# Optimization experiments

Hardware: AMD Instinct MI355X
Metric: run time of the kernel (lower is better)

The kernel has to match this reference:

```python
import jax, jax.numpy as jnp
import numpy as np

LN_EPS = 1e-5  # torch LayerNorm default
MODES = 4


def setup_inputs() -> dict:
    key = jax.random.key(0)
    ks = jax.random.split(key, 5)
    B, S, H = 4, 4096, 1024
    nh, dk = 16, H // 16
    scale = 1.0 / (H * H)
    # frequency mode selection: random shuffle of range(S//2), take 4, sorted (seeded for determinism)
    rng = np.random.default_rng(0)
    index = jnp.asarray(np.sort(rng.permutation(S // 2)[:MODES]).astype(np.int32))
    return {
        "x": jax.random.normal(ks[0], (B, S, H), dtype=jnp.float32),
        "Wq": jax.random.normal(ks[1], (H, H), dtype=jnp.float32) * np.sqrt(2.0 / (H + dk)),
        "bq": jnp.zeros((H,), dtype=jnp.float32),
        "wr": scale * jax.random.uniform(ks[2], (nh, dk, dk, MODES), dtype=jnp.float32),
        "wi": scale * jax.random.uniform(ks[3], (nh, dk, dk, MODES), dtype=jnp.float32),
        "gamma": jnp.ones((H,), dtype=jnp.float32),
        "beta": jnp.zeros((H,), dtype=jnp.float32),
        "index": index,
    }


def reference(x, Wq, bq, wr, wi, gamma, beta, index):
    B, S, H = x.shape
    nh, dk = wr.shape[0], wr.shape[1]
    # q projection and head split: (B,S,H) -> (B,S,nh,dk) -> (B,nh,dk,S)
    q = (x @ Wq.T + bq).reshape(B, S, nh, dk).transpose(0, 2, 3, 1)
    x_ft = jnp.fft.rfft(q, axis=-1)                 # (B,nh,dk,S//2+1) complex
    xm = x_ft[..., index]                           # gather selected modes: (B,nh,dk,M)
    w = wr + 1j * wi                                # (nh,dk,dk,M) complex
    ym = jnp.einsum('bhim,hiom->bhom', xm, w)       # per-mode complex matmul
    # faithful: results written at slots 0..M-1 of out_ft (loop writes out_ft[...,wi])
    out_ft = jnp.zeros((B, nh, dk, S // 2 + 1), dtype=ym.dtype).at[..., :ym.shape[-1]].set(ym)
    x_if = jnp.fft.irfft(out_ft, n=S, axis=-1)      # (B,nh,dk,S) real
    # faithful permute(0,3,2,1).view: flattens as dk-major over heads
    out = x_if.transpose(0, 3, 2, 1).reshape(B, S, H)
    # dropout is identity in eval mode
    y = out + x
    mu = jnp.mean(y, axis=-1, keepdims=True)
    var = jnp.var(y, axis=-1, keepdims=True)
    return (y - mu) * jax.lax.rsqrt(var + LN_EPS) * gamma + beta
```

## Files before the change

### kernel.cpp

```cpp
#include <hip/hip_runtime.h>
#include <math.h>

#define BB 4
#define SS 4096
#define HH 1024
#define NH 16
#define DK 64
#define NMODES 4
#define NSB 64
#define SCHUNK (SS/NSB)
#define PPLANE ((size_t)BB * NSB * HH)
#define TWO_PI 6.28318530717958647692f

__global__ __launch_bounds__(256) void kA_dft(const float* __restrict__ x,
                                              const int* __restrict__ index,
                                              float* __restrict__ P) {
    __shared__ float tab[SCHUNK * 8];
    int t  = threadIdx.x;
    int sb = blockIdx.x & (NSB - 1);
    int b  = blockIdx.x >> 6;

    {
        int sl = t >> 2, m = t & 3;
        int k  = index[m];
        int sv = sb * SCHUNK + sl;
        int r  = (k * sv) & (SS - 1);
        float ang = (float)r * (TWO_PI / (float)SS);
        float sn, cs;
        sincosf(ang, &sn, &cs);
        tab[sl * 8 + m * 2]     = cs;
        tab[sl * 8 + m * 2 + 1] = sn;
    }
    __syncthreads();

    int c0 = t * 4;
    float acc[4][8];
    #pragma unroll
    for (int e = 0; e < 4; ++e)
        #pragma unroll
        for (int q = 0; q < 8; ++q) acc[e][q] = 0.f;

    const float* xp = x + ((size_t)(b * SS + sb * SCHUNK)) * HH + c0;
    #pragma unroll 4
    for (int r = 0; r < SCHUNK; ++r) {
        float4 xv = *(const float4*)(xp + (size_t)r * HH);
        float4 t0 = *(const float4*)&tab[r * 8];
        float4 t1 = *(const float4*)&tab[r * 8 + 4];
        float xe;
        #pragma unroll
        for (int e = 0; e < 4; ++e) {
            xe = (e == 0) ? xv.x : (e == 1) ? xv.y : (e == 2) ? xv.z : xv.w;
            acc[e][0] += xe * t0.x;  acc[e][1] -= xe * t0.y;
            acc[e][2] += xe * t0.z;  acc[e][3] -= xe * t0.w;
            acc[e][4] += xe * t1.x;  acc[e][5] -= xe * t1.y;
            acc[e][6] += xe * t1.z;  acc[e][7] -= xe * t1.w;
        }
    }
    size_t base = (size_t)(b * NSB + sb) * HH + c0;
    #pragma unroll
    for (int q = 0; q < 8; ++q) {
        *(float4*)&P[q * PPLANE + base] =
            make_float4(acc[0][q], acc[1][q], acc[2][q], acc[3][q]);
    }
}

__global__ __launch_bounds__(256) void kA2_reduce(const float* __restrict__ P,
                                                  float* __restrict__ G) {
    int g = blockIdx.x * 256 + threadIdx.x;
    int j = g & (HH - 1);
    int q = (g >> 10) & 7;
    int b = g >> 13;
    float s = 0.f;
    for (int sb = 0; sb < NSB; ++sb)
        s += P[q * PPLANE + (size_t)(b * NSB + sb) * HH + j];
    G[((size_t)(b * HH + j)) * 8 + q] = s;
}

__global__ __launch_bounds__(256) void kB_proj(const float* __restrict__ Wq,
                                               const float* __restrict__ bq,
                                               const int* __restrict__ index,
                                               const float* __restrict__ G,
                                               float* __restrict__ XM) {
    __shared__ float Gs[HH * 8];
    int t = threadIdx.x;
    int cb = blockIdx.x & 15;
    int b  = blockIdx.x >> 4;
    for (int u = t; u < HH * 8; u += 256) Gs[u] = G[(size_t)b * HH * 8 + u];
    __syncthreads();

    int cl = t >> 2, jq = t & 3;
    int c = cb * 64 + cl;
    float acc[8] = {0.f,0.f,0.f,0.f,0.f,0.f,0.f,0.f};
    for (int j0 = jq * 4; j0 < HH; j0 += 16) {
        float4 wv = *(const float4*)&Wq[(size_t)c * HH + j0];
        const float* gp = &Gs[j0 * 8];
        #pragma unroll
        for (int q = 0; q < 8; ++q) acc[q] += wv.x * gp[q];
        #pragma unroll
        for (int q = 0; q < 8; ++q) acc[q] += wv.y * gp[8 + q];
        #pragma unroll
        for (int q = 0; q < 8; ++q) acc[q] += wv.z * gp[16 + q];
        #pragma unroll
        for (int q = 0; q < 8; ++q) acc[q] += wv.w * gp[24 + q];
    }
    #pragma unroll
    for (int q = 0; q < 8; ++q) {
        acc[q] += __shfl_xor(acc[q], 1);
        acc[q] += __shfl_xor(acc[q], 2);
    }
    if (jq == 0) {
        float bias = bq[c];
        #pragma unroll
        for (int m = 0; m < NMODES; ++m)
            if (index[m] == 0) acc[2 * m] += bias * (float)SS;
        float* o = XM + ((size_t)(b * HH + c)) * 8;
        *(float4*)o       = make_float4(acc[0], acc[1], acc[2], acc[3]);
        *(float4*)(o + 4) = make_float4(acc[4], acc[5], acc[6], acc[7]);
    }
}

#define KC_IQ 8
#define KC_II (DK / KC_IQ)
__global__ __launch_bounds__(512) void kC_modes(const float* __restrict__ wr,
                                                const float* __restrict__ wi,
                                                const float* __restrict__ XM,
                                                float* __restrict__ CF) {
    __shared__ float xs[DK * 8];
    __shared__ float red[KC_IQ][DK][9];
    int t = threadIdx.x;
    int o = t & 63, iq = t >> 6;
    int h = blockIdx.x & 15;
    int b = blockIdx.x >> 4;
    for (int u = t; u < DK * 8; u += 512)
        xs[u] = XM[((size_t)(b * HH + h * DK)) * 8 + u];
    __syncthreads();

    float re[4] = {0.f,0.f,0.f,0.f}, im[4] = {0.f,0.f,0.f,0.f};
    #pragma unroll
    for (int ii = 0; ii < KC_II; ++ii) {
        int i = iq * KC_II + ii;
        float4 wrv = *(const float4*)&wr[(((size_t)(h * DK + i)) * DK + o) * 4];
        float4 wiv = *(const float4*)&wi[(((size_t)(h * DK + i)) * DK + o) * 4];
        float xr, xi;
        xr = xs[i * 8 + 0]; xi = xs[i * 8 + 1];
        re[0] += xr * wrv.x - xi * wiv.x;  im[0] += xr * wiv.x + xi * wrv.x;
        xr = xs[i * 8 + 2]; xi = xs[i * 8 + 3];
        re[1] += xr * wrv.y - xi * wiv.y;  im[1] += xr * wiv.y + xi * wrv.y;
        xr = xs[i * 8 + 4]; xi = xs[i * 8 + 5];
        re[2] += xr * wrv.z - xi * wiv.z;  im[2] += xr * wiv.z + xi * wrv.z;
        xr = xs[i * 8 + 6]; xi = xs[i * 8 + 7];
        re[3] += xr * wrv.w - xi * wiv.w;  im[3] += xr * wiv.w + xi * wrv.w;
    }
    #pragma unroll
    for (int m = 0; m < 4; ++m) {
        red[iq][o][2 * m]     = re[m];
        red[iq][o][2 * m + 1] = im[m];
    }
    __syncthreads();
    if (iq == 0) {
        float rr[8];
        #pragma unroll
        for (int q = 0; q < 8; ++q) {
            float s = 0.f;
            #pragma unroll
            for (int g = 0; g < KC_IQ; ++g) s += red[g][o][q];
            rr[q] = s;
        }
        int co = o * NH + h;
        const float inv = 1.0f / (float)SS;
        float* cp = CF + ((size_t)(b * HH + co)) * 8;
        cp[0] =  rr[0] * inv;
        cp[1] =  2.0f * rr[2] * inv;
        cp[2] = -2.0f * rr[3] * inv;
        cp[3] =  2.0f * rr[4] * inv;
        cp[4] = -2.0f * rr[5] * inv;
        cp[5] =  2.0f * rr[6] * inv;
        cp[6] = -2.0f * rr[7] * inv;
        cp[7] =  0.0f;
    }
}

#define KD_ROWS 16
#define KD_RB 8
__global__ __launch_bounds__(256) void kD_out(const float* __restrict__ x,
                                              const float* __restrict__ CF,
                                              const float* __restrict__ gamma,
                                              const float* __restrict__ beta,
                                              float* __restrict__ out) {
    __shared__ float red[4][KD_RB][2];
    int t  = threadIdx.x;
    int b  = blockIdx.x >> 8;
    int s0 = (blockIdx.x & 255) * KD_ROWS;
    int c0 = t * 4;

    const float* cp = CF + (size_t)b * HH * 8 + (size_t)c0 * 8;
    float4 cfa[8];
    #pragma unroll
    for (int e = 0; e < 4; ++e) {
        cfa[2 * e]     = *(const float4*)(cp + e * 8);
        cfa[2 * e + 1] = *(const float4*)(cp + e * 8 + 4);
    }
    float4 g4 = *(const float4*)&gamma[c0];
    float4 b4 = *(const float4*)&beta[c0];
    int w = t >> 6, lane = t & 63;

    for (int batch = 0; batch < KD_ROWS / KD_RB; ++batch) {
        float y[KD_RB][4], sm[KD_RB], sq[KD_RB];
        #pragma unroll
        for (int r = 0; r < KD_RB; ++r) {
            int s = s0 + batch * KD_RB + r;
            float ang = (float)s * (TWO_PI / (float)SS);
            float s1, c1;
            sincosf(ang, &s1, &c1);
            float c2 = c1 * c1 - s1 * s1, s2 = 2.f * s1 * c1;
            float c3 = c2 * c1 - s2 * s1, s3 = s2 * c1 + c2 * s1;

            float4 xv = *(const float4*)&x[((size_t)(b * SS + s)) * HH + c0];
            #pragma unroll
            for (int e = 0; e < 4; ++e) {
                float xe = (e == 0) ? xv.x : (e == 1) ? xv.y : (e == 2) ? xv.z : xv.w;
                float4 A = cfa[2 * e], Bv = cfa[2 * e + 1];
                y[r][e] = xe + A.x + A.y * c1 + A.z * s1 + A.w * c2
                             + Bv.x * s2 + Bv.y * c3 + Bv.z * s3;
            }
            sm[r] = y[r][0] + y[r][1] + y[r][2] + y[r][3];
            sq[r] = y[r][0]*y[r][0] + y[r][1]*y[r][1]
                  + y[r][2]*y[r][2] + y[r][3]*y[r][3];
        }
        #pragma unroll
        for (int off = 1; off < 64; off <<= 1) {
            #pragma unroll
            for (int r = 0; r < KD_RB; ++r) {
                sm[r] += __shfl_xor(sm[r], off);
                sq[r] += __shfl_xor(sq[r], off);
            }
        }
        if (lane == 0) {
            #pragma unroll
            for (int r = 0; r < KD_RB; ++r) {
                red[w][r][0] = sm[r];
                red[w][r][1] = sq[r];
            }
        }
        __syncthreads();
        #pragma unroll
        for (int r = 0; r < KD_RB; ++r) {
            int s = s0 + batch * KD_RB + r;
            float tot  = red[0][r][0] + red[1][r][0] + red[2][r][0] + red[3][r][0];
            float totq = red[0][r][1] + red[1][r][1] + red[2][r][1] + red[3][r][1];
            float mean = tot * (1.0f / (float)HH);
            float var  = totq * (1.0f / (float)HH) - mean * mean;
            float rs = rsqrtf(var + 1e-5f);
            float4 o4;
            o4.x = (y[r][0] - mean) * rs * g4.x + b4.x;
            o4.y = (y[r][1] - mean) * rs * g4.y + b4.y;
            o4.z = (y[r][2] - mean) * rs * g4.z + b4.z;
            o4.w = (y[r][3] - mean) * rs * g4.w + b4.w;
            *(float4*)&out[((size_t)(b * SS + s)) * HH + c0] = o4;
        }
        __syncthreads();
    }
}

extern "C" void kernel_launch(void* const* d_in, const int* in_sizes, int n_in,
                              void* d_out, int out_size, void* d_ws, size_t ws_size,
                              hipStream_t stream) {
    const float* x     = (const float*)d_in[0];
    const float* Wq    = (const float*)d_in[1];
    const float* bq    = (const float*)d_in[2];
    const float* wr    = (const float*)d_in[3];
    const float* wi    = (const float*)d_in[4];
    const float* gamma = (const float*)d_in[5];
    const float* beta  = (const float*)d_in[6];
    const int*   index = (const int*)d_in[7];
    float* out = (float*)d_out;
    float* ws  = (float*)d_ws;

    const size_t nP     = PPLANE * 8;
    const size_t nSmall = (size_t)BB * HH * 8;

    float *P, *G, *XM, *CF;
    if (ws_size >= (nP + 3 * nSmall) * sizeof(float)) {
        P  = ws;
        G  = P + nP;
        XM = G + nSmall;
        CF = XM + nSmall;
    } else {
        P  = out;
        G  = ws;
        XM = G + nSmall;
        CF = XM + nSmall;
    }

    hipLaunchKernelGGL(kA_dft,     dim3(BB * NSB), dim3(256), 0, stream, x, index, P);
    hipLaunchKernelGGL(kA2_reduce, dim3(BB * HH * 8 / 256), dim3(256), 0, stream, P, G);
    hipLaunchKernelGGL(kB_proj,    dim3(BB * 16), dim3(256), 0, stream, Wq, bq, index, G, XM);
    hipLaunchKernelGGL(kC_modes,   dim3(BB * NH), dim3(512), 0, stream, wr, wi, XM, CF);
    hipLaunchKernelGGL(kD_out,     dim3(BB * (SS / KD_ROWS)), dim3(256), 0, stream, x, CF, gamma, beta, out);
}
```

Before: 68.32 us.

## Double DFT split blocks, widen projection grid, and precompute row trig in LayerNorm kernel

Raises the number of sequence chunks in the partial-DFT kernel so more blocks fill the GPU, and changes the G layout to mode-plane-major so the reduce writes coalesced and the projection reads float4 from shared memory. The projection kernel gets four times as many blocks, each with 16 threads per output column and wider shuffle reductions. The output kernel computes sincos once per row into shared memory and issues all x loads of a batch before the arithmetic to increase memory-level parallelism. The trade-off is a larger partial buffer P that the reduce must stream, plus extra shuffles per projection output.

```diff
diff --git a/kernel.cpp b/kernel.cpp
--- a/kernel.cpp
+++ b/kernel.cpp
@@ -7,7 +7,7 @@
 #define NH 16
 #define DK 64
 #define NMODES 4
-#define NSB 64
+#define NSB 128
 #define SCHUNK (SS/NSB)
 #define PPLANE ((size_t)BB * NSB * HH)
 #define TWO_PI 6.28318530717958647692f
@@ -18,9 +18,9 @@
     __shared__ float tab[SCHUNK * 8];
     int t  = threadIdx.x;
     int sb = blockIdx.x & (NSB - 1);
-    int b  = blockIdx.x >> 6;
-
-    {
+    int b  = blockIdx.x >> 7;
+
+    if (t < SCHUNK * NMODES) {
         int sl = t >> 2, m = t & 3;
         int k  = index[m];
         int sv = sb * SCHUNK + sl;
@@ -70,10 +70,12 @@
     int j = g & (HH - 1);
     int q = (g >> 10) & 7;
     int b = g >> 13;
+    const float* pp = P + q * PPLANE + (size_t)b * NSB * HH + j;
     float s = 0.f;
+    #pragma unroll 16
     for (int sb = 0; sb < NSB; ++sb)
-        s += P[q * PPLANE + (size_t)(b * NSB + sb) * HH + j];
-    G[((size_t)(b * HH + j)) * 8 + q] = s;
+        s += pp[(size_t)sb * HH];
+    G[g] = s;
 }
 
 __global__ __launch_bounds__(256) void kB_proj(const float* __restrict__ Wq,
@@ -81,32 +83,34 @@
                                                const int* __restrict__ index,
                                                const float* __restrict__ G,
                                                float* __restrict__ XM) {
-    __shared__ float Gs[HH * 8];
-    int t = threadIdx.x;
-    int cb = blockIdx.x & 15;
-    int b  = blockIdx.x >> 4;
-    for (int u = t; u < HH * 8; u += 256) Gs[u] = G[(size_t)b * HH * 8 + u];
-    __syncthreads();
-
-    int cl = t >> 2, jq = t & 3;
-    int c = cb * 64 + cl;
+    __shared__ float Gs[8 * HH];
+    int t  = threadIdx.x;
+    int cb = blockIdx.x & 63;
+    int b  = blockIdx.x >> 6;
+    {
+        const float4* gsrc = (const float4*)(G + (size_t)b * 8 * HH);
+        float4* gdst = (float4*)Gs;
+        for (int u = t; u < 2 * HH; u += 256) gdst[u] = gsrc[u];
+    }
+    __syncthreads();
+
+    int cl = t >> 4, jq = t & 15;
+    int c = cb * 16 + cl;
     float acc[8] = {0.f,0.f,0.f,0.f,0.f,0.f,0.f,0.f};
-    for (int j0 = jq * 4; j0 < HH; j0 += 16) {
+    for (int j0 = jq * 4; j0 < HH; j0 += 64) {
         float4 wv = *(const float4*)&Wq[(size_t)c * HH + j0];
-        const float* gp = &Gs[j0 * 8];
-        #pragma unroll
-        for (int q = 0; q < 8; ++q) acc[q] += wv.x * gp[q];
-        #pragma unroll
-        for (int q = 0; q < 8; ++q) acc[q] += wv.y * gp[8 + q];
-        #pragma unroll
-        for (int q = 0; q < 8; ++q) acc[q] += wv.z * gp[16 + q];
-        #pragma unroll
-        for (int q = 0; q < 8; ++q) acc[q] += wv.w * gp[24 + q];
+        #pragma unroll
+        for (int q = 0; q < 8; ++q) {
+            float4 gv = *(const float4*)&Gs[q * HH + j0];
+            acc[q] += wv.x * gv.x + wv.y * gv.y + wv.z * gv.z + wv.w * gv.w;
+        }
     }
     #pragma unroll
     for (int q = 0; q < 8; ++q) {
         acc[q] += __shfl_xor(acc[q], 1);
         acc[q] += __shfl_xor(acc[q], 2);
+        acc[q] += __shfl_xor(acc[q], 4);
+        acc[q] += __shfl_xor(acc[q], 8);
     }
     if (jq == 0) {
         float bias = bq[c];
@@ -187,12 +191,21 @@
                                               const float* __restrict__ gamma,
                                               const float* __restrict__ beta,
                                               float* __restrict__ out) {
+    __shared__ float trig[KD_ROWS][2];
     __shared__ float red[4][KD_RB][2];
     int t  = threadIdx.x;
     int b  = blockIdx.x >> 8;
     int s0 = (blockIdx.x & 255) * KD_ROWS;
     int c0 = t * 4;
 
+    if (t < KD_ROWS) {
+        float ang = (float)(s0 + t) * (TWO_PI / (float)SS);
+        float sn, cs;
+        sincosf(ang, &sn, &cs);
+        trig[t][0] = cs;
+        trig[t][1] = sn;
+    }
+
     const float* cp = CF + (size_t)b * HH * 8 + (size_t)c0 * 8;
     float4 cfa[8];
     #pragma unroll
@@ -203,29 +216,34 @@
     float4 g4 = *(const float4*)&gamma[c0];
     float4 b4 = *(const float4*)&beta[c0];
     int w = t >> 6, lane = t & 63;
+    __syncthreads();
 
     for (int batch = 0; batch < KD_ROWS / KD_RB; ++batch) {
-        float y[KD_RB][4], sm[KD_RB], sq[KD_RB];
+        float4 yv[KD_RB];
         #pragma unroll
         for (int r = 0; r < KD_RB; ++r) {
             int s = s0 + batch * KD_RB + r;
-            float ang = (float)s * (TWO_PI / (float)SS);
-            float s1, c1;
-            sincosf(ang, &s1, &c1);
+            yv[r] = *(const float4*)&x[((size_t)(b * SS + s)) * HH + c0];
+        }
+        float sm[KD_RB], sq[KD_RB];
+        #pragma unroll
+        for (int r = 0; r < KD_RB; ++r) {
+            int ri = batch * KD_RB + r;
+            float c1 = trig[ri][0], s1 = trig[ri][1];
             float c2 = c1 * c1 - s1 * s1, s2 = 2.f * s1 * c1;
             float c3 = c2 * c1 - s2 * s1, s3 = s2 * c1 + c2 * s1;
-
-            float4 xv = *(const float4*)&x[((size_t)(b * SS + s)) * HH + c0];
+            float ye[4];
             #pragma unroll
             for (int e = 0; e < 4; ++e) {
-                float xe = (e == 0) ? xv.x : (e == 1) ? xv.y : (e == 2) ? xv.z : xv.w;
+                float xe = (e == 0) ? yv[r].x : (e == 1) ? yv[r].y
+                         : (e == 2) ? yv[r].z : yv[r].w;
                 float4 A = cfa[2 * e], Bv = cfa[2 * e + 1];
-                y[r][e] = xe + A.x + A.y * c1 + A.z * s1 + A.w * c2
-                             + Bv.x * s2 + Bv.y * c3 + Bv.z * s3;
+                ye[e] = xe + A.x + A.y * c1 + A.z * s1 + A.w * c2
+                           + Bv.x * s2 + Bv.y * c3 + Bv.z * s3;
             }
-            sm[r] = y[r][0] + y[r][1] + y[r][2] + y[r][3];
-            sq[r] = y[r][0]*y[r][0] + y[r][1]*y[r][1]
-                  + y[r][2]*y[r][2] + y[r][3]*y[r][3];
+            yv[r] = make_float4(ye[0], ye[1], ye[2], ye[3]);
+            sm[r] = ye[0] + ye[1] + ye[2] + ye[3];
+            sq[r] = ye[0]*ye[0] + ye[1]*ye[1] + ye[2]*ye[2] + ye[3]*ye[3];
         }
         #pragma unroll
         for (int off = 1; off < 64; off <<= 1) {
@@ -252,10 +270,10 @@
             float var  = totq * (1.0f / (float)HH) - mean * mean;
             float rs = rsqrtf(var + 1e-5f);
             float4 o4;
-            o4.x = (y[r][0] - mean) * rs * g4.x + b4.x;
-            o4.y = (y[r][1] - mean) * rs * g4.y + b4.y;
-            o4.z = (y[r][2] - mean) * rs * g4.z + b4.z;
-            o4.w = (y[r][3] - mean) * rs * g4.w + b4.w;
+            o4.x = (yv[r].x - mean) * rs * g4.x + b4.x;
+            o4.y = (yv[r].y - mean) * rs * g4.y + b4.y;
+            o4.z = (yv[r].z - mean) * rs * g4.z + b4.z;
+            o4.w = (yv[r].w - mean) * rs * g4.w + b4.w;
             *(float4*)&out[((size_t)(b * SS + s)) * HH + c0] = o4;
         }
         __syncthreads();
@@ -294,7 +312,7 @@
 
     hipLaunchKernelGGL(kA_dft,     dim3(BB * NSB), dim3(256), 0, stream, x, index, P);
     hipLaunchKernelGGL(kA2_reduce, dim3(BB * HH * 8 / 256), dim3(256), 0, stream, P, G);
-    hipLaunchKernelGGL(kB_proj,    dim3(BB * 16), dim3(256), 0, stream, Wq, bq, index, G, XM);
+    hipLaunchKernelGGL(kB_proj,    dim3(BB * 64), dim3(256), 0, stream, Wq, bq, index, G, XM);
     hipLaunchKernelGGL(kC_modes,   dim3(BB * NH), dim3(512), 0, stream, wr, wi, XM, CF);
     hipLaunchKernelGGL(kD_out,     dim3(BB * (SS / KD_ROWS)), dim3(256), 0, stream, x, CF, gamma, beta, out);
 }
```

Measured after the change: 61.73 us. -9.6%, faster.
